# Kernel optimization log

Measured on AMD Instinct MI355X. Metric: run time of the kernel, lower is better.

The kernel has to match this reference:

```python
import jax, jax.numpy as jnp
import numpy as np

B, L, DK, DV, H = 2, 2048, 512, 512, 8
DH_K = DK // H  # 64
DH_V = DV // H  # 64


def setup_inputs() -> dict:
    key = jax.random.key(0)
    ks = jax.random.split(key, 6)
    scale_w = 1.0 / np.sqrt(DK)
    return {
        "keys": jax.random.normal(ks[0], (B, L, DK), dtype=jnp.float32),
        "queries": jax.random.normal(ks[1], (B, L, DK), dtype=jnp.float32),
        "values": jax.random.normal(ks[2], (B, L, DV), dtype=jnp.float32),
        "WQ": jax.random.normal(ks[3], (H, DK, DH_K), dtype=jnp.float32) * scale_w,
        "WK": jax.random.normal(ks[4], (H, DK, DH_K), dtype=jnp.float32) * scale_w,
        "WV": jax.random.normal(ks[5], (H, DV, DH_V), dtype=jnp.float32) * scale_w,
    }


def reference(keys, queries, values, WQ, WK, WV):
    # Per-head projections, vectorized over all H heads at once.
    Q = jnp.einsum('bld,hde->bhle', queries, WQ)   # [B,H,Lq,dh]
    K = jnp.einsum('bld,hde->bhle', keys, WK)      # [B,H,Lk,dh]
    V = jnp.einsum('bld,hde->bhle', values, WV)    # [B,H,Lk,dv_h]
    Lk = keys.shape[1]
    # NOTE: original scales by sqrt(seq_len_k), not sqrt(head_dim).
    y = jnp.einsum('bhqe,bhke->bhqk', Q, K) / jnp.sqrt(jnp.float32(Lk))
    # NOTE: original applies softmax over torch dim=1 of [B,Lq,Lk],
    # i.e. the QUERY axis (axis=2 here in [B,H,Lq,Lk]).
    z = jax.nn.softmax(y, axis=2)
    out = jnp.einsum('bhqk,bhke->bhqe', z, V)      # [B,H,Lq,dv_h]
    # Concat heads on the feature dim (same order as torch.concat(..., 2)).
    Bq, Hh, Lq, Dh = out.shape
    return out.transpose(0, 2, 1, 3).reshape(Bq, Lq, Hh * Dh)
```

## Files before the change

### kernel.cpp

```cpp
#include <hip/hip_runtime.h>
#include <hip/hip_bf16.h>

#define LL 2048
#define DM 512
#define SCALE2 0.031879357f

typedef unsigned short u16;
typedef __attribute__((ext_vector_type(8))) short short8;
typedef __attribute__((ext_vector_type(4))) short short4v;
typedef __attribute__((ext_vector_type(4))) float f32x4;

#define XAQ_OFF 0u
#define XAK_OFF 2097152u
#define XAV_OFF 4194304u
#define WB_OFF  6291456u
#define QA_OFF  7077888u
#define KA_OFF  9175040u
#define VB_OFF  11272192u
#define S_OFF   13369344u

__device__ __forceinline__ unsigned pk2(float lo, float hi) {
  union { __hip_bfloat162 h2; unsigned u; } v;
  v.h2.x = __float2bfloat16(lo);
  v.h2.y = __float2bfloat16(hi);
  return v.u;
}
__device__ __forceinline__ size_t frag_idx(int bh, int t64, int w, int c, int lane) {
  return ((((size_t)(bh * 32 + t64) * 4 + w) * 2 + c) * 64 + lane) * 8;
}
__device__ __forceinline__ size_t vb8_idx(int bh, int kt2, int w, int et, int lane) {
  return ((((size_t)(bh * 16 + kt2) * 4 + w) * 4 + et) * 64 + lane) * 8;
}

__global__ __launch_bounds__(256) void prep_kernel(
    const float* __restrict__ queries, const float* __restrict__ keys,
    const float* __restrict__ values, const float* __restrict__ WQ,
    const float* __restrict__ WK, const float* __restrict__ WV,
    u16* __restrict__ wsb) {
  int t = threadIdx.x;
  int blk = blockIdx.x;
  if (blk < 768) {
    int tens = blk >> 8;
    int grp  = blk & 255;
    const float* src = (tens == 0 ? queries : tens == 1 ? keys : values) +
                       (size_t)grp * 16 * 512;
    __shared__ __align__(16) u16 Xs[16][520];
#pragma unroll
    for (int rep = 0; rep < 8; ++rep) {
      int f4 = t + rep * 256;
      int row = f4 >> 7, c4 = f4 & 127;
      float4 v = *(const float4*)(src + (size_t)row * 512 + c4 * 4);
      union { unsigned u[2]; short4v s; } o;
      o.u[0] = pk2(v.x, v.y);
      o.u[1] = pk2(v.z, v.w);
      *(short4v*)&Xs[row][c4 * 4] = o.s;
    }
    __syncthreads();
    u16* dst = wsb + (tens == 0 ? XAQ_OFF : tens == 1 ? XAK_OFF : XAV_OFF) +
               (size_t)grp * 16 * 64 * 8;
#pragma unroll
    for (int rep = 0; rep < 4; ++rep) {
      int o = t + rep * 256;
      int kt = o >> 6, lane = o & 63;
      int quad = lane >> 4, l16 = lane & 15;
      short8 v = *(const short8*)&Xs[l16][kt * 32 + quad * 8];
      *(short8*)(dst + (size_t)o * 8) = v;
    }
  } else {
    int c2 = (blk - 768) * 256 + t;
    int lane = c2 & 63;
    int nt = (c2 >> 6) & 3;
    int kt = (c2 >> 8) & 15;
    int h  = (c2 >> 12) & 7;
    int z  = c2 >> 15;
    int quad = lane >> 4, l16 = lane & 15;
    const float* W = (z == 0) ? WQ : (z == 1) ? WK : WV;
    const float* src = W + ((size_t)h * DM + kt * 32 + quad * 8) * 64 + nt * 16 + l16;
    float f[8];
#pragma unroll
    for (int j = 0; j < 8; ++j) f[j] = src[(size_t)j * 64];
    union { unsigned u[4]; short8 s; } o;
#pragma unroll
    for (int j = 0; j < 4; ++j) o.u[j] = pk2(f[2 * j], f[2 * j + 1]);
    *(short8*)(wsb + WB_OFF + (size_t)c2 * 8) = o.s;
  }
}

__global__ __launch_bounds__(256) void proj_kernel(u16* __restrict__ wsb) {
  int t = threadIdx.x;
  int lane = t & 63, w = t >> 6, quad = lane >> 4, l16 = lane & 15;
  int z = blockIdx.z, bh = blockIdx.y, b = bh >> 3, h = bh & 7;
  int QT = blockIdx.x;

  const u16* Bw = wsb + WB_OFF + ((size_t)(z * 8 + h) * 16) * 4 * 64 * 8;
  const u16* Ab = wsb + (z == 0 ? XAQ_OFF : z == 1 ? XAK_OFF : XAV_OFF) +
      (((size_t)b * 128 + QT * 4 + w) * 16) * 64 * 8;

  f32x4 acc[4];
#pragma unroll
  for (int nt = 0; nt < 4; ++nt) acc[nt] = (f32x4){0.f, 0.f, 0.f, 0.f};

#pragma unroll 4
  for (int kt = 0; kt < 16; ++kt) {
    short8 a = *(const short8*)(Ab + ((size_t)kt * 64 + lane) * 8);
#pragma unroll
    for (int nt = 0; nt < 4; ++nt) {
      short8 bb = *(const short8*)(Bw + (((size_t)kt * 4 + nt) * 64 + lane) * 8);
      acc[nt] = __builtin_amdgcn_mfma_f32_16x16x32_bf16(a, bb, acc[nt], 0, 0, 0);
    }
  }

  __shared__ float Cs[64][68];
  float sc = (z == 0) ? SCALE2 : 1.0f;
#pragma unroll
  for (int nt = 0; nt < 4; ++nt)
#pragma unroll
    for (int r = 0; r < 4; ++r)
      Cs[w * 16 + quad * 4 + r][nt * 16 + l16] = acc[nt][r] * sc;
  __syncthreads();

  if (z < 2) {
    u16* base = wsb + (z == 0 ? QA_OFF : KA_OFF);
#pragma unroll
    for (int c = 0; c < 2; ++c) {
      const float* srcr = &Cs[w * 16 + l16][c * 32 + quad * 8];
      union { unsigned u[4]; short8 s; } o;
#pragma unroll
      for (int j = 0; j < 4; ++j) o.u[j] = pk2(srcr[2 * j], srcr[2 * j + 1]);
      *(short8*)(base + frag_idx(bh, QT, w, c, lane)) = o.s;
    }
  } else {
#pragma unroll
    for (int et = 0; et < 4; ++et) {
      union { unsigned u[2]; short4v s; } o;
      o.u[0] = pk2(Cs[w * 16 + quad * 4 + 0][et * 16 + l16],
                   Cs[w * 16 + quad * 4 + 1][et * 16 + l16]);
      o.u[1] = pk2(Cs[w * 16 + quad * 4 + 2][et * 16 + l16],
                   Cs[w * 16 + quad * 4 + 3][et * 16 + l16]);
      *(short4v*)(wsb + VB_OFF + vb8_idx(bh, QT >> 1, w, et, lane) + (QT & 1) * 4) = o.s;
    }
  }
}

#define STATS_PHASE(QB0, QB1, QNEW)                                             \
  {                                                                             \
    _Pragma("unroll")                                                           \
    for (int mt = 0; mt < 4; ++mt) {                                            \
      f32x4 y = (f32x4){0.f, 0.f, 0.f, 0.f};                                    \
      __builtin_amdgcn_s_setprio(1);                                            \
      y = __builtin_amdgcn_mfma_f32_16x16x32_bf16(ka[mt][0], QB0, y, 0, 0, 0);  \
      y = __builtin_amdgcn_mfma_f32_16x16x32_bf16(ka[mt][1], QB1, y, 0, 0, 0);  \
      __builtin_amdgcn_s_setprio(0);                                            \
      _Pragma("unroll")                                                         \
      for (int r = 0; r < 4; ++r) rs[mt][r] += __builtin_amdgcn_exp2f(y[r]);    \
    }                                                                           \
    QB0 = *(const short8*)(wsb + QA_OFF + frag_idx(bh, (QNEW) & 31, w, 0, lane)); \
    QB1 = *(const short8*)(wsb + QA_OFF + frag_idx(bh, (QNEW) & 31, w, 1, lane)); \
  }

__global__ __launch_bounds__(256) void stats_kernel(u16* __restrict__ wsb) {
  int t = threadIdx.x;
  int lane = t & 63, w = t >> 6, quad = lane >> 4, l16 = lane & 15;
  int bh = blockIdx.x;
  int KT = blockIdx.y;

  short8 ka[4][2];
#pragma unroll
  for (int mt = 0; mt < 4; ++mt)
#pragma unroll
    for (int c = 0; c < 2; ++c)
      ka[mt][c] = *(const short8*)(wsb + KA_OFF + frag_idx(bh, KT, mt, c, lane));

  float rs[4][4];
#pragma unroll
  for (int mt = 0; mt < 4; ++mt)
#pragma unroll
    for (int r = 0; r < 4; ++r) rs[mt][r] = 0.f;

  short8 qA0 = *(const short8*)(wsb + QA_OFF + frag_idx(bh, 0, w, 0, lane));
  short8 qA1 = *(const short8*)(wsb + QA_OFF + frag_idx(bh, 0, w, 1, lane));
  short8 qB0 = *(const short8*)(wsb + QA_OFF + frag_idx(bh, 1, w, 0, lane));
  short8 qB1 = *(const short8*)(wsb + QA_OFF + frag_idx(bh, 1, w, 1, lane));
  short8 qC0 = *(const short8*)(wsb + QA_OFF + frag_idx(bh, 2, w, 0, lane));
  short8 qC1 = *(const short8*)(wsb + QA_OFF + frag_idx(bh, 2, w, 1, lane));

#pragma unroll 1
  for (int j = 0; j < 10; ++j) {
    int k0 = 3 * j;
    STATS_PHASE(qA0, qA1, k0 + 3);
    STATS_PHASE(qB0, qB1, k0 + 4);
    STATS_PHASE(qC0, qC1, k0 + 5);
  }
  STATS_PHASE(qA0, qA1, 0);
  STATS_PHASE(qB0, qB1, 0);

#pragma unroll
  for (int mt = 0; mt < 4; ++mt)
#pragma unroll
    for (int r = 0; r < 4; ++r) {
      rs[mt][r] += __shfl_xor(rs[mt][r], 1);
      rs[mt][r] += __shfl_xor(rs[mt][r], 2);
      rs[mt][r] += __shfl_xor(rs[mt][r], 4);
      rs[mt][r] += __shfl_xor(rs[mt][r], 8);
    }

  __shared__ float Sred[4][64];
  if (l16 == 0) {
#pragma unroll
    for (int mt = 0; mt < 4; ++mt)
#pragma unroll
      for (int r = 0; r < 4; ++r)
        Sred[w][mt * 16 + quad * 4 + r] = rs[mt][r];
  }
  __syncthreads();
  if (t < 64) {
    float s = Sred[0][t] + Sred[1][t] + Sred[2][t] + Sred[3][t];
    float* S = (float*)(wsb + S_OFF);
    S[(size_t)bh * LL + KT * 64 + t] = 1.0f / s;
  }
}

#define ATTN_PHASE(KE0, KE1, KO0, KO1, VBX, S4E, S4O, KNEW)                         \
  {                                                                                 \
    _Pragma("unroll")                                                               \
    for (int nt = 0; nt < 4; ++nt) {                                                \
      f32x4 ye = (f32x4){0.f, 0.f, 0.f, 0.f};                                       \
      f32x4 yo = (f32x4){0.f, 0.f, 0.f, 0.f};                                       \
      __builtin_amdgcn_s_setprio(1);                                                \
      ye = __builtin_amdgcn_mfma_f32_16x16x32_bf16(KE0, qf[nt][0], ye, 0, 0, 0);    \
      ye = __builtin_amdgcn_mfma_f32_16x16x32_bf16(KE1, qf[nt][1], ye, 0, 0, 0);    \
      yo = __builtin_amdgcn_mfma_f32_16x16x32_bf16(KO0, qf[nt][0], yo, 0, 0, 0);    \
      yo = __builtin_amdgcn_mfma_f32_16x16x32_bf16(KO1, qf[nt][1], yo, 0, 0, 0);    \
      __builtin_amdgcn_s_setprio(0);                                                \
      union { unsigned u[4]; short8 s; } pc;                                        \
      pc.u[0] = pk2(__builtin_amdgcn_exp2f(ye[0]) * S4E.x,                          \
                    __builtin_amdgcn_exp2f(ye[1]) * S4E.y);                         \
      pc.u[1] = pk2(__builtin_amdgcn_exp2f(ye[2]) * S4E.z,                          \
                    __builtin_amdgcn_exp2f(ye[3]) * S4E.w);                         \
      pc.u[2] = pk2(__builtin_amdgcn_exp2f(yo[0]) * S4O.x,                          \
                    __builtin_amdgcn_exp2f(yo[1]) * S4O.y);                         \
      pc.u[3] = pk2(__builtin_amdgcn_exp2f(yo[2]) * S4O.z,                          \
                    __builtin_amdgcn_exp2f(yo[3]) * S4O.w);                         \
      short8 pa8 = pc.s;                                                            \
      __builtin_amdgcn_s_setprio(1);                                                \
      _Pragma("unroll")                                                             \
      for (int et = 0; et < 4; ++et)                                                \
        oacc[nt][et] = __builtin_amdgcn_mfma_f32_16x16x32_bf16(pa8, VBX[et],        \
                                                               oacc[nt][et], 0, 0, 0); \
      __builtin_amdgcn_s_setprio(0);                                                \
    }                                                                               \
    {                                                                               \
      int ke = (2 * (KNEW)) & 31, ko = (2 * (KNEW) + 1) & 31, kv = (KNEW) & 15;     \
      KE0 = *(const short8*)(wsb + KA_OFF + frag_idx(bh, ke, w, 0, lane));          \
      KE1 = *(const short8*)(wsb + KA_OFF + frag_idx(bh, ke, w, 1, lane));          \
      KO0 = *(const short8*)(wsb + KA_OFF + frag_idx(bh, ko, w, 0, lane));          \
      KO1 = *(const short8*)(wsb + KA_OFF + frag_idx(bh, ko, w, 1, lane));          \
      _Pragma("unroll")                                                             \
      for (int et = 0; et < 4; ++et)                                                \
        VBX[et] = *(const short8*)(wsb + VB_OFF + vb8_idx(bh, kv, w, et, lane));    \
      S4E = *(const float4*)(S + ke * 64 + w * 16 + quad * 4);                      \
      S4O = *(const float4*)(S + ko * 64 + w * 16 + quad * 4);                      \
    }                                                                               \
  }

#define ATTN_LOADSET(KE0, KE1, KO0, KO1, VBX, S4E, S4O, KT2)                        \
  {                                                                                 \
    int ke = 2 * (KT2), ko = 2 * (KT2) + 1;                                         \
    KE0 = *(const short8*)(wsb + KA_OFF + frag_idx(bh, ke, w, 0, lane));            \
    KE1 = *(const short8*)(wsb + KA_OFF + frag_idx(bh, ke, w, 1, lane));            \
    KO0 = *(const short8*)(wsb + KA_OFF + frag_idx(bh, ko, w, 0, lane));            \
    KO1 = *(const short8*)(wsb + KA_OFF + frag_idx(bh, ko, w, 1, lane));            \
    _Pragma("unroll")                                                               \
    for (int et = 0; et < 4; ++et)                                                  \
      VBX[et] = *(const short8*)(wsb + VB_OFF + vb8_idx(bh, (KT2), w, et, lane));   \
    S4E = *(const float4*)(S + ke * 64 + w * 16 + quad * 4);                        \
    S4O = *(const float4*)(S + ko * 64 + w * 16 + quad * 4);                        \
  }

__global__ __launch_bounds__(256, 2) void attn_kernel(const u16* __restrict__ wsb,
                                                      float* __restrict__ out) {
  int t = threadIdx.x;
  int lane = t & 63, w = t >> 6, quad = lane >> 4, l16 = lane & 15;
  int bh = blockIdx.x, b = bh >> 3, h = bh & 7;
  int QT = blockIdx.y, qbase = QT * 64;
  const float* S = (const float*)(wsb + S_OFF) + (size_t)bh * LL;

  short8 qf[4][2];
#pragma unroll
  for (int nt = 0; nt < 4; ++nt)
#pragma unroll
    for (int c = 0; c < 2; ++c)
      qf[nt][c] = *(const short8*)(wsb + QA_OFF + frag_idx(bh, QT, nt, c, lane));

  f32x4 oacc[4][4];
#pragma unroll
  for (int nt = 0; nt < 4; ++nt)
#pragma unroll
    for (int et = 0; et < 4; ++et) oacc[nt][et] = (f32x4){0.f, 0.f, 0.f, 0.f};

  short8 aKE0, aKE1, aKO0, aKO1, aVB[4]; float4 aSE, aSO;
  short8 bKE0, bKE1, bKO0, bKO1, bVB[4]; float4 bSE, bSO;
  short8 cKE0, cKE1, cKO0, cKO1, cVB[4]; float4 cSE, cSO;
  ATTN_LOADSET(aKE0, aKE1, aKO0, aKO1, aVB, aSE, aSO, 0)
  ATTN_LOADSET(bKE0, bKE1, bKO0, bKO1, bVB, bSE, bSO, 1)
  ATTN_LOADSET(cKE0, cKE1, cKO0, cKO1, cVB, cSE, cSO, 2)

#pragma unroll 1
  for (int j = 0; j < 5; ++j) {
    int k0 = 3 * j;
    ATTN_PHASE(aKE0, aKE1, aKO0, aKO1, aVB, aSE, aSO, k0 + 3)
    ATTN_PHASE(bKE0, bKE1, bKO0, bKO1, bVB, bSE, bSO, k0 + 4)
    ATTN_PHASE(cKE0, cKE1, cKO0, cKO1, cVB, cSE, cSO, k0 + 5)
  }
  ATTN_PHASE(aKE0, aKE1, aKO0, aKO1, aVB, aSE, aSO, 0)

  __shared__ float red[4][64][68];
#pragma unroll
  for (int nt = 0; nt < 4; ++nt)
#pragma unroll
    for (int et = 0; et < 4; ++et)
#pragma unroll
      for (int r = 0; r < 4; ++r)
        red[w][nt * 16 + quad * 4 + r][et * 16 + l16] = oacc[nt][et][r];
  __syncthreads();
  float* og = out + ((size_t)b * LL + qbase + w * 16) * 512 + h * 64;
#pragma unroll
  for (int i = 0; i < 16; ++i) {
    float s = red[0][w * 16 + i][lane] + red[1][w * 16 + i][lane] +
              red[2][w * 16 + i][lane] + red[3][w * 16 + i][lane];
    og[(size_t)i * 512 + lane] = s;
  }
}

extern "C" void kernel_launch(void* const* d_in, const int* in_sizes, int n_in,
                              void* d_out, int out_size, void* d_ws, size_t ws_size,
                              hipStream_t stream) {
  const float* keys    = (const float*)d_in[0];
  const float* queries = (const float*)d_in[1];
  const float* values  = (const float*)d_in[2];
  const float* WQ      = (const float*)d_in[3];
  const float* WK      = (const float*)d_in[4];
  const float* WV      = (const float*)d_in[5];
  float* out = (float*)d_out;
  u16* wsb = (u16*)d_ws;

  prep_kernel<<<dim3(1152), 256, 0, stream>>>(queries, keys, values, WQ, WK, WV, wsb);
  proj_kernel<<<dim3(32, 16, 3), 256, 0, stream>>>(wsb);
  stats_kernel<<<dim3(16, 32), 256, 0, stream>>>(wsb);
  attn_kernel<<<dim3(16, 32), 256, 0, stream>>>(wsb, out);
}
```

Baseline: 135.0 us.

## Double block size in stats and attention kernels to share loads across wave groups

Stats and attention kernels now launch 512-thread blocks, each covering two 64-row tiles (two key tiles for stats, two query tiles for attention) with two groups of four waves. The two groups read the same Q or K/V fragments at the same time, which may improve cache reuse and halves the grid. The attention epilogue reuses the shared reduction buffer in two passes with extra barriers. The cost is fewer blocks (256 instead of 512) and higher register and occupancy pressure per CU.

```diff
diff --git a/kernel.cpp b/kernel.cpp
--- a/kernel.cpp
+++ b/kernel.cpp
@@ -154,15 +154,17 @@
       _Pragma("unroll")                                                         \
       for (int r = 0; r < 4; ++r) rs[mt][r] += __builtin_amdgcn_exp2f(y[r]);    \
     }                                                                           \
-    QB0 = *(const short8*)(wsb + QA_OFF + frag_idx(bh, (QNEW) & 31, w, 0, lane)); \
-    QB1 = *(const short8*)(wsb + QA_OFF + frag_idx(bh, (QNEW) & 31, w, 1, lane)); \
-  }
-
-__global__ __launch_bounds__(256) void stats_kernel(u16* __restrict__ wsb) {
+    QB0 = *(const short8*)(wsb + QA_OFF + frag_idx(bh, (QNEW) & 31, w4q, 0, lane)); \
+    QB1 = *(const short8*)(wsb + QA_OFF + frag_idx(bh, (QNEW) & 31, w4q, 1, lane)); \
+  }
+
+__global__ __launch_bounds__(512, 2) void stats_kernel(u16* __restrict__ wsb) {
   int t = threadIdx.x;
-  int lane = t & 63, w = t >> 6, quad = lane >> 4, l16 = lane & 15;
+  int lane = t & 63, wave = t >> 6, quad = lane >> 4, l16 = lane & 15;
+  int w4q = wave & 3;
+  int m2  = wave >> 2;
   int bh = blockIdx.x;
-  int KT = blockIdx.y;
+  int KT = blockIdx.y * 2 + m2;
 
   short8 ka[4][2];
 #pragma unroll
@@ -177,12 +179,12 @@
 #pragma unroll
     for (int r = 0; r < 4; ++r) rs[mt][r] = 0.f;
 
-  short8 qA0 = *(const short8*)(wsb + QA_OFF + frag_idx(bh, 0, w, 0, lane));
-  short8 qA1 = *(const short8*)(wsb + QA_OFF + frag_idx(bh, 0, w, 1, lane));
-  short8 qB0 = *(const short8*)(wsb + QA_OFF + frag_idx(bh, 1, w, 0, lane));
-  short8 qB1 = *(const short8*)(wsb + QA_OFF + frag_idx(bh, 1, w, 1, lane));
-  short8 qC0 = *(const short8*)(wsb + QA_OFF + frag_idx(bh, 2, w, 0, lane));
-  short8 qC1 = *(const short8*)(wsb + QA_OFF + frag_idx(bh, 2, w, 1, lane));
+  short8 qA0 = *(const short8*)(wsb + QA_OFF + frag_idx(bh, 0, w4q, 0, lane));
+  short8 qA1 = *(const short8*)(wsb + QA_OFF + frag_idx(bh, 0, w4q, 1, lane));
+  short8 qB0 = *(const short8*)(wsb + QA_OFF + frag_idx(bh, 1, w4q, 0, lane));
+  short8 qB1 = *(const short8*)(wsb + QA_OFF + frag_idx(bh, 1, w4q, 1, lane));
+  short8 qC0 = *(const short8*)(wsb + QA_OFF + frag_idx(bh, 2, w4q, 0, lane));
+  short8 qC1 = *(const short8*)(wsb + QA_OFF + frag_idx(bh, 2, w4q, 1, lane));
 
 #pragma unroll 1
   for (int j = 0; j < 10; ++j) {
@@ -204,19 +206,19 @@
       rs[mt][r] += __shfl_xor(rs[mt][r], 8);
     }
 
-  __shared__ float Sred[4][64];
+  __shared__ float Sred[4][128];
   if (l16 == 0) {
 #pragma unroll
     for (int mt = 0; mt < 4; ++mt)
 #pragma unroll
       for (int r = 0; r < 4; ++r)
-        Sred[w][mt * 16 + quad * 4 + r] = rs[mt][r];
+        Sred[w4q][m2 * 64 + mt * 16 + quad * 4 + r] = rs[mt][r];
   }
   __syncthreads();
-  if (t < 64) {
+  if (t < 128) {
     float s = Sred[0][t] + Sred[1][t] + Sred[2][t] + Sred[3][t];
     float* S = (float*)(wsb + S_OFF);
-    S[(size_t)bh * LL + KT * 64 + t] = 1.0f / s;
+    S[(size_t)bh * LL + blockIdx.y * 128 + t] = 1.0f / s;
   }
 }
 
@@ -251,38 +253,40 @@
     }                                                                               \
     {                                                                               \
       int ke = (2 * (KNEW)) & 31, ko = (2 * (KNEW) + 1) & 31, kv = (KNEW) & 15;     \
-      KE0 = *(const short8*)(wsb + KA_OFF + frag_idx(bh, ke, w, 0, lane));          \
-      KE1 = *(const short8*)(wsb + KA_OFF + frag_idx(bh, ke, w, 1, lane));          \
-      KO0 = *(const short8*)(wsb + KA_OFF + frag_idx(bh, ko, w, 0, lane));          \
-      KO1 = *(const short8*)(wsb + KA_OFF + frag_idx(bh, ko, w, 1, lane));          \
+      KE0 = *(const short8*)(wsb + KA_OFF + frag_idx(bh, ke, w4, 0, lane));         \
+      KE1 = *(const short8*)(wsb + KA_OFF + frag_idx(bh, ke, w4, 1, lane));         \
+      KO0 = *(const short8*)(wsb + KA_OFF + frag_idx(bh, ko, w4, 0, lane));         \
+      KO1 = *(const short8*)(wsb + KA_OFF + frag_idx(bh, ko, w4, 1, lane));         \
       _Pragma("unroll")                                                             \
       for (int et = 0; et < 4; ++et)                                                \
-        VBX[et] = *(const short8*)(wsb + VB_OFF + vb8_idx(bh, kv, w, et, lane));    \
-      S4E = *(const float4*)(S + ke * 64 + w * 16 + quad * 4);                      \
-      S4O = *(const float4*)(S + ko * 64 + w * 16 + quad * 4);                      \
+        VBX[et] = *(const short8*)(wsb + VB_OFF + vb8_idx(bh, kv, w4, et, lane));   \
+      S4E = *(const float4*)(S + ke * 64 + w4 * 16 + quad * 4);                     \
+      S4O = *(const float4*)(S + ko * 64 + w4 * 16 + quad * 4);                     \
     }                                                                               \
   }
 
 #define ATTN_LOADSET(KE0, KE1, KO0, KO1, VBX, S4E, S4O, KT2)                        \
   {                                                                                 \
     int ke = 2 * (KT2), ko = 2 * (KT2) + 1;                                         \
-    KE0 = *(const short8*)(wsb + KA_OFF + frag_idx(bh, ke, w, 0, lane));            \
-    KE1 = *(const short8*)(wsb + KA_OFF + frag_idx(bh, ke, w, 1, lane));            \
-    KO0 = *(const short8*)(wsb + KA_OFF + frag_idx(bh, ko, w, 0, lane));            \
-    KO1 = *(const short8*)(wsb + KA_OFF + frag_idx(bh, ko, w, 1, lane));            \
+    KE0 = *(const short8*)(wsb + KA_OFF + frag_idx(bh, ke, w4, 0, lane));           \
+    KE1 = *(const short8*)(wsb + KA_OFF + frag_idx(bh, ke, w4, 1, lane));           \
+    KO0 = *(const short8*)(wsb + KA_OFF + frag_idx(bh, ko, w4, 0, lane));           \
+    KO1 = *(const short8*)(wsb + KA_OFF + frag_idx(bh, ko, w4, 1, lane));           \
     _Pragma("unroll")                                                               \
     for (int et = 0; et < 4; ++et)                                                  \
-      VBX[et] = *(const short8*)(wsb + VB_OFF + vb8_idx(bh, (KT2), w, et, lane));   \
-    S4E = *(const float4*)(S + ke * 64 + w * 16 + quad * 4);                        \
-    S4O = *(const float4*)(S + ko * 64 + w * 16 + quad * 4);                        \
-  }
-
-__global__ __launch_bounds__(256, 2) void attn_kernel(const u16* __restrict__ wsb,
+      VBX[et] = *(const short8*)(wsb + VB_OFF + vb8_idx(bh, (KT2), w4, et, lane));  \
+    S4E = *(const float4*)(S + ke * 64 + w4 * 16 + quad * 4);                       \
+    S4O = *(const float4*)(S + ko * 64 + w4 * 16 + quad * 4);                       \
+  }
+
+__global__ __launch_bounds__(512, 2) void attn_kernel(const u16* __restrict__ wsb,
                                                       float* __restrict__ out) {
   int t = threadIdx.x;
-  int lane = t & 63, w = t >> 6, quad = lane >> 4, l16 = lane & 15;
+  int lane = t & 63, wave = t >> 6, quad = lane >> 4, l16 = lane & 15;
+  int w4 = wave & 3;
+  int n2 = wave >> 2;
   int bh = blockIdx.x, b = bh >> 3, h = bh & 7;
-  int QT = blockIdx.y, qbase = QT * 64;
+  int QT2 = blockIdx.y;
   const float* S = (const float*)(wsb + S_OFF) + (size_t)bh * LL;
 
   short8 qf[4][2];
@@ -290,7 +294,7 @@
   for (int nt = 0; nt < 4; ++nt)
 #pragma unroll
     for (int c = 0; c < 2; ++c)
-      qf[nt][c] = *(const short8*)(wsb + QA_OFF + frag_idx(bh, QT, nt, c, lane));
+      qf[nt][c] = *(const short8*)(wsb + QA_OFF + frag_idx(bh, QT2 * 2 + n2, nt, c, lane));
 
   f32x4 oacc[4][4];
 #pragma unroll
@@ -315,20 +319,27 @@
   ATTN_PHASE(aKE0, aKE1, aKO0, aKO1, aVB, aSE, aSO, 0)
 
   __shared__ float red[4][64][68];
-#pragma unroll
-  for (int nt = 0; nt < 4; ++nt)
-#pragma unroll
-    for (int et = 0; et < 4; ++et)
-#pragma unroll
-      for (int r = 0; r < 4; ++r)
-        red[w][nt * 16 + quad * 4 + r][et * 16 + l16] = oacc[nt][et][r];
-  __syncthreads();
-  float* og = out + ((size_t)b * LL + qbase + w * 16) * 512 + h * 64;
-#pragma unroll
-  for (int i = 0; i < 16; ++i) {
-    float s = red[0][w * 16 + i][lane] + red[1][w * 16 + i][lane] +
-              red[2][w * 16 + i][lane] + red[3][w * 16 + i][lane];
-    og[(size_t)i * 512 + lane] = s;
+#pragma unroll 1
+  for (int cc = 0; cc < 2; ++cc) {
+    if (cc) __syncthreads();
+    if (n2 == cc) {
+#pragma unroll
+      for (int nt = 0; nt < 4; ++nt)
+#pragma unroll
+        for (int et = 0; et < 4; ++et)
+#pragma unroll
+          for (int r = 0; r < 4; ++r)
+            red[w4][nt * 16 + quad * 4 + r][et * 16 + l16] = oacc[nt][et][r];
+    }
+    __syncthreads();
+    float* og = out + ((size_t)b * LL + QT2 * 128 + cc * 64 + wave * 8) * 512 + h * 64;
+#pragma unroll
+    for (int i = 0; i < 8; ++i) {
+      int row = wave * 8 + i;
+      float s = red[0][row][lane] + red[1][row][lane] +
+                red[2][row][lane] + red[3][row][lane];
+      og[(size_t)i * 512 + lane] = s;
+    }
   }
 }
 
@@ -346,6 +357,6 @@
 
   prep_kernel<<<dim3(1152), 256, 0, stream>>>(queries, keys, values, WQ, WK, WV, wsb);
   proj_kernel<<<dim3(32, 16, 3), 256, 0, stream>>>(wsb);
-  stats_kernel<<<dim3(16, 32), 256, 0, stream>>>(wsb);
-  attn_kernel<<<dim3(16, 32), 256, 0, stream>>>(wsb, out);
-}
+  stats_kernel<<<dim3(16, 16), 512, 0, stream>>>(wsb);
+  attn_kernel<<<dim3(16, 16), 512, 0, stream>>>(wsb, out);
+}
```

Result: no change. 135.4 us (+0.3%).

## Fuse fp32-to-bf16 input conversion into projection kernel via shared memory

Applied to the files above, without the earlier changes.

Each projection block now loads its own 64-row fp32 slice of queries, keys or values, converts it to bf16 in shared memory and reads A fragments from there. The prep kernel only converts the weights. This removes the round trip of writing and re-reading bf16 activations through global memory. In exchange, each fp32 input tile is reread by all 8 head blocks, which raises global read traffic. A 66KB shared buffer (unioned with the output staging) also limits occupancy.

```diff
diff --git a/kernel.cpp b/kernel.cpp
--- a/kernel.cpp
+++ b/kernel.cpp
@@ -10,9 +10,6 @@
 typedef __attribute__((ext_vector_type(4))) short short4v;
 typedef __attribute__((ext_vector_type(4))) float f32x4;
 
-#define XAQ_OFF 0u
-#define XAK_OFF 2097152u
-#define XAV_OFF 4194304u
 #define WB_OFF  6291456u
 #define QA_OFF  7077888u
 #define KA_OFF  9175040u
@@ -33,68 +30,54 @@
 }
 
 __global__ __launch_bounds__(256) void prep_kernel(
+    const float* __restrict__ WQ, const float* __restrict__ WK,
+    const float* __restrict__ WV, u16* __restrict__ wsb) {
+  int c2 = blockIdx.x * 256 + threadIdx.x;
+  int lane = c2 & 63;
+  int nt = (c2 >> 6) & 3;
+  int kt = (c2 >> 8) & 15;
+  int h  = (c2 >> 12) & 7;
+  int z  = c2 >> 15;
+  int quad = lane >> 4, l16 = lane & 15;
+  const float* W = (z == 0) ? WQ : (z == 1) ? WK : WV;
+  const float* src = W + ((size_t)h * DM + kt * 32 + quad * 8) * 64 + nt * 16 + l16;
+  float f[8];
+#pragma unroll
+  for (int j = 0; j < 8; ++j) f[j] = src[(size_t)j * 64];
+  union { unsigned u[4]; short8 s; } o;
+#pragma unroll
+  for (int j = 0; j < 4; ++j) o.u[j] = pk2(f[2 * j], f[2 * j + 1]);
+  *(short8*)(wsb + WB_OFF + (size_t)c2 * 8) = o.s;
+}
+
+__global__ __launch_bounds__(256) void proj_kernel(
     const float* __restrict__ queries, const float* __restrict__ keys,
-    const float* __restrict__ values, const float* __restrict__ WQ,
-    const float* __restrict__ WK, const float* __restrict__ WV,
-    u16* __restrict__ wsb) {
-  int t = threadIdx.x;
-  int blk = blockIdx.x;
-  if (blk < 768) {
-    int tens = blk >> 8;
-    int grp  = blk & 255;
-    const float* src = (tens == 0 ? queries : tens == 1 ? keys : values) +
-                       (size_t)grp * 16 * 512;
-    __shared__ __align__(16) u16 Xs[16][520];
-#pragma unroll
-    for (int rep = 0; rep < 8; ++rep) {
-      int f4 = t + rep * 256;
-      int row = f4 >> 7, c4 = f4 & 127;
-      float4 v = *(const float4*)(src + (size_t)row * 512 + c4 * 4);
-      union { unsigned u[2]; short4v s; } o;
-      o.u[0] = pk2(v.x, v.y);
-      o.u[1] = pk2(v.z, v.w);
-      *(short4v*)&Xs[row][c4 * 4] = o.s;
-    }
-    __syncthreads();
-    u16* dst = wsb + (tens == 0 ? XAQ_OFF : tens == 1 ? XAK_OFF : XAV_OFF) +
-               (size_t)grp * 16 * 64 * 8;
-#pragma unroll
-    for (int rep = 0; rep < 4; ++rep) {
-      int o = t + rep * 256;
-      int kt = o >> 6, lane = o & 63;
-      int quad = lane >> 4, l16 = lane & 15;
-      short8 v = *(const short8*)&Xs[l16][kt * 32 + quad * 8];
-      *(short8*)(dst + (size_t)o * 8) = v;
-    }
-  } else {
-    int c2 = (blk - 768) * 256 + t;
-    int lane = c2 & 63;
-    int nt = (c2 >> 6) & 3;
-    int kt = (c2 >> 8) & 15;
-    int h  = (c2 >> 12) & 7;
-    int z  = c2 >> 15;
-    int quad = lane >> 4, l16 = lane & 15;
-    const float* W = (z == 0) ? WQ : (z == 1) ? WK : WV;
-    const float* src = W + ((size_t)h * DM + kt * 32 + quad * 8) * 64 + nt * 16 + l16;
-    float f[8];
-#pragma unroll
-    for (int j = 0; j < 8; ++j) f[j] = src[(size_t)j * 64];
-    union { unsigned u[4]; short8 s; } o;
-#pragma unroll
-    for (int j = 0; j < 4; ++j) o.u[j] = pk2(f[2 * j], f[2 * j + 1]);
-    *(short8*)(wsb + WB_OFF + (size_t)c2 * 8) = o.s;
-  }
-}
-
-__global__ __launch_bounds__(256) void proj_kernel(u16* __restrict__ wsb) {
+    const float* __restrict__ values, u16* __restrict__ wsb) {
   int t = threadIdx.x;
   int lane = t & 63, w = t >> 6, quad = lane >> 4, l16 = lane & 15;
   int z = blockIdx.z, bh = blockIdx.y, b = bh >> 3, h = bh & 7;
   int QT = blockIdx.x;
 
+  __shared__ __align__(16) union {
+    u16   Xs[64][520];
+    float Cs[64][68];
+  } sm;
+
+  const float* xsrc = (z == 0 ? queries : z == 1 ? keys : values) +
+                      ((size_t)b * LL + QT * 64) * 512;
+#pragma unroll
+  for (int rep = 0; rep < 32; ++rep) {
+    int f4 = t + rep * 256;
+    int row = f4 >> 7, c4 = f4 & 127;
+    float4 v = *(const float4*)(xsrc + (size_t)row * 512 + c4 * 4);
+    union { unsigned u[2]; short4v s; } o;
+    o.u[0] = pk2(v.x, v.y);
+    o.u[1] = pk2(v.z, v.w);
+    *(short4v*)&sm.Xs[row][c4 * 4] = o.s;
+  }
+  __syncthreads();
+
   const u16* Bw = wsb + WB_OFF + ((size_t)(z * 8 + h) * 16) * 4 * 64 * 8;
-  const u16* Ab = wsb + (z == 0 ? XAQ_OFF : z == 1 ? XAK_OFF : XAV_OFF) +
-      (((size_t)b * 128 + QT * 4 + w) * 16) * 64 * 8;
 
   f32x4 acc[4];
 #pragma unroll
@@ -102,28 +85,28 @@
 
 #pragma unroll 4
   for (int kt = 0; kt < 16; ++kt) {
-    short8 a = *(const short8*)(Ab + ((size_t)kt * 64 + lane) * 8);
+    short8 a = *(const short8*)&sm.Xs[w * 16 + l16][kt * 32 + quad * 8];
 #pragma unroll
     for (int nt = 0; nt < 4; ++nt) {
       short8 bb = *(const short8*)(Bw + (((size_t)kt * 4 + nt) * 64 + lane) * 8);
       acc[nt] = __builtin_amdgcn_mfma_f32_16x16x32_bf16(a, bb, acc[nt], 0, 0, 0);
     }
   }
-
-  __shared__ float Cs[64][68];
+  __syncthreads();
+
   float sc = (z == 0) ? SCALE2 : 1.0f;
 #pragma unroll
   for (int nt = 0; nt < 4; ++nt)
 #pragma unroll
     for (int r = 0; r < 4; ++r)
-      Cs[w * 16 + quad * 4 + r][nt * 16 + l16] = acc[nt][r] * sc;
+      sm.Cs[w * 16 + quad * 4 + r][nt * 16 + l16] = acc[nt][r] * sc;
   __syncthreads();
 
   if (z < 2) {
     u16* base = wsb + (z == 0 ? QA_OFF : KA_OFF);
 #pragma unroll
     for (int c = 0; c < 2; ++c) {
-      const float* srcr = &Cs[w * 16 + l16][c * 32 + quad * 8];
+      const float* srcr = &sm.Cs[w * 16 + l16][c * 32 + quad * 8];
       union { unsigned u[4]; short8 s; } o;
 #pragma unroll
       for (int j = 0; j < 4; ++j) o.u[j] = pk2(srcr[2 * j], srcr[2 * j + 1]);
@@ -133,10 +116,10 @@
 #pragma unroll
     for (int et = 0; et < 4; ++et) {
       union { unsigned u[2]; short4v s; } o;
-      o.u[0] = pk2(Cs[w * 16 + quad * 4 + 0][et * 16 + l16],
-                   Cs[w * 16 + quad * 4 + 1][et * 16 + l16]);
-      o.u[1] = pk2(Cs[w * 16 + quad * 4 + 2][et * 16 + l16],
-                   Cs[w * 16 + quad * 4 + 3][et * 16 + l16]);
+      o.u[0] = pk2(sm.Cs[w * 16 + quad * 4 + 0][et * 16 + l16],
+                   sm.Cs[w * 16 + quad * 4 + 1][et * 16 + l16]);
+      o.u[1] = pk2(sm.Cs[w * 16 + quad * 4 + 2][et * 16 + l16],
+                   sm.Cs[w * 16 + quad * 4 + 3][et * 16 + l16]);
       *(short4v*)(wsb + VB_OFF + vb8_idx(bh, QT >> 1, w, et, lane) + (QT & 1) * 4) = o.s;
     }
   }
@@ -344,8 +327,8 @@
   float* out = (float*)d_out;
   u16* wsb = (u16*)d_ws;
 
-  prep_kernel<<<dim3(1152), 256, 0, stream>>>(queries, keys, values, WQ, WK, WV, wsb);
-  proj_kernel<<<dim3(32, 16, 3), 256, 0, stream>>>(wsb);
+  prep_kernel<<<dim3(384), 256, 0, stream>>>(WQ, WK, WV, wsb);
+  proj_kernel<<<dim3(32, 16, 3), 256, 0, stream>>>(queries, keys, values, wsb);
   stats_kernel<<<dim3(16, 32), 256, 0, stream>>>(wsb);
   attn_kernel<<<dim3(16, 32), 256, 0, stream>>>(wsb, out);
 }
```

Result: slower. 146.9 us (+8.8%).
